# Optimization experiments

Measured on AMD Instinct MI355X. Metric: run time of the kernel, lower is better.

## Reference

```python
import jax, jax.numpy as jnp
import numpy as np

RWKV_K_CLAMP = 60.0
B, T, C = 8, 1024, 1024
LAYER_ID, N_LAYER = 2, 12


def _decay_speed():
    # replicate RWKV_TimeMix.__init__ decay_speed construction
    first = 1
    f1 = 3.0 + (LAYER_ID - first) / (N_LAYER - 1 - first) * (1.2 - 3.0)
    f2 = 0.65 + (LAYER_ID - first) / (N_LAYER - 1 - first) * (0.4 - 0.65)
    if LAYER_ID == first:
        f1 += 0.5
    if LAYER_ID == N_LAYER - 2:
        f2 = 0.4
    if LAYER_ID == N_LAYER - 1:
        f2 = 0.37
    h = np.arange(C, dtype=np.float64)
    return (f2 ** (h / (C - 1) * 7.0)) * f1


def setup_inputs() -> dict:
    key = jax.random.key(0)
    ks = jax.random.split(key, 6)
    scale = 1.0 / np.sqrt(C)
    time_mix = np.ones((C,), np.float32)
    time_mix[: C // 2] = 0.0
    return {
        "x": jax.random.normal(ks[0], (B, T, C), jnp.float32),
        "time_decay": jnp.asarray(np.log(_decay_speed()), jnp.float32),  # (C,)
        "time_first": jnp.full((C,), np.log(0.3), jnp.float32),
        "time_mix": jnp.asarray(time_mix),
        "combined_mix": jnp.full((C,), 0.01, jnp.float32),
        "Wk": jax.random.normal(ks[1], (C, C), jnp.float32) * scale,
        "Wv": jax.random.normal(ks[2], (C, C), jnp.float32) * scale,
        "Wr": jax.random.normal(ks[3], (C, C), jnp.float32) * scale,
        "Wo": jax.random.normal(ks[4], (C, C), jnp.float32) * scale,
    }


def _wkv(w, u, k, v):
    # w,u: (C,); k,v: (B,T,C). Numerically-stable decayed linear recurrence
    # (RWKV wkv kernel: running-max, like online softmax).
    b = k.shape[0]
    init = (
        jnp.zeros((b, C), k.dtype),            # numerator state a
        jnp.zeros((b, C), k.dtype),            # denominator state b
        jnp.full((b, C), -1e38, k.dtype),      # running max exponent p
    )

    def step(carry, kv):
        a, bb, p = carry
        kt, vt = kv  # (B,C)
        no = jnp.maximum(p, u + kt)
        e1 = jnp.exp(p - no)
        e2 = jnp.exp(u + kt - no)
        y = (e1 * a + e2 * vt) / (e1 * bb + e2)
        no2 = jnp.maximum(w + p, kt)
        e1 = jnp.exp(w + p - no2)
        e2 = jnp.exp(kt - no2)
        return (e1 * a + e2 * vt, e1 * bb + e2, no2), y

    _, y = jax.lax.scan(step, init, (k.transpose(1, 0, 2), v.transpose(1, 0, 2)))
    return y.transpose(1, 0, 2)  # (B,T,C)


def reference(x, time_decay, time_first, time_mix, combined_mix, Wk, Wv, Wr, Wo):
    b, t, c = x.shape
    zrow = jnp.zeros((b, 1, c), x.dtype)
    x_m1 = jnp.concatenate([zrow, x[:, :-1, :]], axis=1)   # time_shift / x_{t-1}
    x_p1 = jnp.concatenate([x[:, 1:, :], zrow], axis=1)    # x_{t+1}
    half = c // 2
    x_comb = jnp.concatenate([x_m1[:, :, :half], x_p1[:, :, half:]], axis=-1)
    xm = x * time_mix + x_m1 * (1.0 - time_mix) + x_comb * combined_mix
    k = jnp.exp(jnp.minimum(jnp.einsum("btc,dc->btd", xm, Wk), RWKV_K_CLAMP))
    v = jnp.einsum("btc,dc->btd", xm, Wv)
    r = jnp.einsum("btc,dc->btd", xm, Wr)
    wkv = _wkv(time_decay / t, time_first / t, k, v)
    return jnp.einsum("btc,dc->btd", jax.nn.sigmoid(r) * wkv, Wo)
```

## Files before the change

### kernel.cpp

```cpp
#include <hip/hip_runtime.h>
#include <hip/hip_bf16.h>
#include <stdint.h>

#define B_SZ 8
#define T_LEN 1024
#define C_DIM 1024
#define M_ROWS (B_SZ * T_LEN)
#define NCH 32
#define CHL (T_LEN / NCH)

typedef unsigned short ushort_t;
typedef __attribute__((ext_vector_type(8))) short short8;
typedef __attribute__((ext_vector_type(4))) float f32x4;
typedef __attribute__((ext_vector_type(4))) unsigned short us4;

static __device__ __forceinline__ float bf2f(ushort_t u) {
  union { unsigned int i; float f; } x; x.i = ((unsigned int)u) << 16; return x.f;
}
static __device__ __forceinline__ ushort_t f2bf(float f) {
  union { float f; unsigned int i; } x; x.f = f;
  unsigned int r = x.i + 0x7fffu + ((x.i >> 16) & 1u);
  return (ushort_t)(r >> 16);
}

static __device__ __forceinline__ void gload_lds16(const void* g, void* l) {
  __builtin_amdgcn_global_load_lds(
      (const __attribute__((address_space(1))) void*)g,
      (__attribute__((address_space(3))) void*)l, 16, 0, 0);
}

__global__ void cvt_w_kernel(const float* __restrict__ wk, const float* __restrict__ wv,
                             const float* __restrict__ wr, const float* __restrict__ wo,
                             ushort_t* __restrict__ out) {
  int gid = blockIdx.x * 256 + threadIdx.x;
  int which = gid >> 18;
  int off = (gid << 2) & ((1 << 20) - 1);
  const float* src = which == 0 ? wk : which == 1 ? wv : which == 2 ? wr : wo;
  float4 v = *(const float4*)(src + off);
  us4 o = {f2bf(v.x), f2bf(v.y), f2bf(v.z), f2bf(v.w)};
  *(us4*)(out + (size_t)gid * 4) = o;
}

__global__ void xm_kernel(const float* __restrict__ x, const float* __restrict__ tm,
                          const float* __restrict__ cm, ushort_t* __restrict__ xmb) {
  int gid = blockIdx.x * 256 + threadIdx.x;
  int c4 = (gid & (C_DIM / 4 - 1)) * 4;
  int t = (gid >> 8) & (T_LEN - 1);
  const float4 zero = {0.f, 0.f, 0.f, 0.f};
  float4 xv = *(const float4*)(x + (size_t)gid * 4);
  float4 xp = (t > 0) ? *(const float4*)(x + (size_t)gid * 4 - C_DIM) : zero;
  float4 xn = (t < T_LEN - 1) ? *(const float4*)(x + (size_t)gid * 4 + C_DIM) : zero;
  float4 tmv = *(const float4*)(tm + c4);
  float4 cmv = *(const float4*)(cm + c4);
  float4 xc = (c4 < C_DIM / 2) ? xp : xn;
  us4 o;
  o.x = f2bf(xv.x * tmv.x + xp.x * (1.f - tmv.x) + xc.x * cmv.x);
  o.y = f2bf(xv.y * tmv.y + xp.y * (1.f - tmv.y) + xc.y * cmv.y);
  o.z = f2bf(xv.z * tmv.z + xp.z * (1.f - tmv.z) + xc.z * cmv.z);
  o.w = f2bf(xv.w * tmv.w + xp.w * (1.f - tmv.w) + xc.w * cmv.w);
  *(us4*)(xmb + (size_t)gid * 4) = o;
}

__global__ __launch_bounds__(256, 3) void gemm_fused(const ushort_t* __restrict__ A,
                                                     const ushort_t* __restrict__ Bw,
                                                     ushort_t* __restrict__ outK,
                                                     ushort_t* __restrict__ outV,
                                                     ushort_t* __restrict__ outR) {
  constexpr int K = 1024;
  constexpr int NT = K / 32;
  __shared__ ushort_t As[3][128 * 32];
  __shared__ ushort_t Bs[3][128 * 32];

  const int tid = threadIdx.x;
  const int lane = tid & 63;
  const int wave = tid >> 6;

  const int bid = blockIdx.x;
  const int xcd = bid & 7;
  const int r = bid >> 3;
  const int bm = (xcd * 8 + (r & 7)) * 128;
  const int jb = r >> 3;
  const int mode = jb >> 3;
  const int bn = (jb & 7) * 128;
  const ushort_t* Bp = Bw + ((size_t)mode << 20);

  const int wr = (wave >> 1) * 64;
  const int wc = (wave & 1) * 64;

  f32x4 acc[4][4];
#pragma unroll
  for (int m = 0; m < 4; ++m)
#pragma unroll
    for (int n = 0; n < 4; ++n) acc[m][n] = (f32x4){0.f, 0.f, 0.f, 0.f};

  const int srow = tid >> 2;
  const int scol = (((tid & 3) ^ ((srow >> 1) & 3)) * 8);
  const ushort_t* Ag = A + (size_t)(bm + srow) * K + scol;
  const ushort_t* Bg = Bp + (size_t)(bn + srow) * K + scol;

  const int fr = lane & 15;
  const int kq = lane >> 4;
  const int ps = (kq ^ ((fr >> 1) & 3)) * 8;

  auto stage = [&](int buf, int k0) {
    ushort_t* ap = &As[buf][tid * 8];
    ushort_t* bp = &Bs[buf][tid * 8];
    gload_lds16(Ag + k0, ap);
    gload_lds16(Ag + (size_t)64 * K + k0, ap + 64 * 32);
    gload_lds16(Bg + k0, bp);
    gload_lds16(Bg + (size_t)64 * K + k0, bp + 64 * 32);
  };

  stage(0, 0);
  stage(1, 32);
  asm volatile("s_waitcnt vmcnt(4)" ::: "memory");
  __builtin_amdgcn_s_barrier();
  __builtin_amdgcn_sched_barrier(0);

  int cur = 0, nxt2 = 2;
#pragma unroll 1
  for (int t = 0; t < NT; ++t) {
    if (t + 2 < NT) stage(nxt2, (t + 2) * 32);
    const ushort_t* asb = &As[cur][0];
    const ushort_t* bsb = &Bs[cur][0];
    short8 af[4], bfr[4];
#pragma unroll
    for (int m = 0; m < 4; ++m)
      af[m] = *(const short8*)&asb[(wr + m * 16 + fr) * 32 + ps];
#pragma unroll
    for (int n = 0; n < 4; ++n)
      bfr[n] = *(const short8*)&bsb[(wc + n * 16 + fr) * 32 + ps];
#pragma unroll
    for (int m = 0; m < 4; ++m)
#pragma unroll
      for (int n = 0; n < 4; ++n)
        acc[m][n] = __builtin_amdgcn_mfma_f32_16x16x32_bf16(af[m], bfr[n], acc[m][n], 0, 0, 0);
    if (t + 2 < NT) {
      asm volatile("s_waitcnt vmcnt(4)" ::: "memory");
    } else {
      asm volatile("s_waitcnt vmcnt(0)" ::: "memory");
    }
    __builtin_amdgcn_s_barrier();
    __builtin_amdgcn_sched_barrier(0);
    cur = (cur == 2) ? 0 : cur + 1;
    nxt2 = (nxt2 == 2) ? 0 : nxt2 + 1;
  }

#pragma unroll
  for (int m = 0; m < 4; ++m)
#pragma unroll
    for (int n = 0; n < 4; ++n)
#pragma unroll
      for (int j = 0; j < 4; ++j) {
        float v = acc[m][n][j];
        size_t idx = (size_t)(bm + wr + m * 16 + kq * 4 + j) * C_DIM + (bn + wc + n * 16 + fr);
        if (mode == 0) {
          outK[idx] = f2bf(__expf(fminf(v, 60.f)));
        } else if (mode == 1) {
          outV[idx] = f2bf(v);
        } else {
          outR[idx] = f2bf(1.f / (1.f + __expf(-v)));
        }
      }
}

__global__ __launch_bounds__(256, 2) void gemm_out(const ushort_t* __restrict__ A,
                                                   const ushort_t* __restrict__ Bw,
                                                   float* __restrict__ outF) {
  constexpr int K = 1024;
  constexpr int NT = K / 64;
  __shared__ ushort_t As[2][128 * 64];
  __shared__ ushort_t Bs[2][128 * 64];

  const int tid = threadIdx.x;
  const int l = tid & 63;
  const int wave = tid >> 6;
  const int fr = l & 15;
  const int kq = l >> 4;

  const int bid = blockIdx.x;
  const int xcd = bid & 7;
  const int idx = bid >> 3;
  const int jb = idx >> 3;
  const int bm = (xcd * 8 + (idx & 7)) * 128;
  const int bn = jb * 128;

  const int wr = (wave >> 1) * 64;
  const int wc = (wave & 1) * 64;

  f32x4 acc[4][4];
#pragma unroll
  for (int m = 0; m < 4; ++m)
#pragma unroll
    for (int n = 0; n < 4; ++n) acc[m][n] = (f32x4){0.f, 0.f, 0.f, 0.f};

  int srow[4], scol[4];
#pragma unroll
  for (int j = 0; j < 4; ++j) {
    int row = wave * 32 + j * 8 + (l >> 3);
    srow[j] = row;
    scol[j] = ((l & 7) ^ (row & 7)) * 8;
  }
  const ushort_t* AgB = A + (size_t)bm * K;
  const ushort_t* BgB = Bw + (size_t)bn * K;
  const int dst0 = wave * 2048 + l * 8;

  auto stage = [&](int buf, int k0) {
#pragma unroll
    for (int j = 0; j < 4; ++j)
      gload_lds16(AgB + (size_t)srow[j] * K + scol[j] + k0, &As[buf][dst0 + j * 512]);
#pragma unroll
    for (int j = 0; j < 4; ++j)
      gload_lds16(BgB + (size_t)srow[j] * K + scol[j] + k0, &Bs[buf][dst0 + j * 512]);
  };

  stage(0, 0);
  asm volatile("s_waitcnt vmcnt(0)" ::: "memory");
  __syncthreads();

  const int ps0 = ((0 * 4 + kq) ^ (fr & 7)) * 8;
  const int ps1 = ((1 * 4 + kq) ^ (fr & 7)) * 8;

  int cur = 0;
  for (int t = 0; t < NT; ++t) {
    if (t < NT - 1) stage(cur ^ 1, (t + 1) * 64);
    short8 af[4][2], bfr[4][2];
#pragma unroll
    for (int m = 0; m < 4; ++m) {
      af[m][0] = *(const short8*)&As[cur][(wr + m * 16 + fr) * 64 + ps0];
      af[m][1] = *(const short8*)&As[cur][(wr + m * 16 + fr) * 64 + ps1];
    }
#pragma unroll
    for (int n = 0; n < 4; ++n) {
      bfr[n][0] = *(const short8*)&Bs[cur][(wc + n * 16 + fr) * 64 + ps0];
      bfr[n][1] = *(const short8*)&Bs[cur][(wc + n * 16 + fr) * 64 + ps1];
    }
#pragma unroll
    for (int m = 0; m < 4; ++m)
#pragma unroll
      for (int n = 0; n < 4; ++n)
#pragma unroll
        for (int ks = 0; ks < 2; ++ks)
          acc[m][n] = __builtin_amdgcn_mfma_f32_16x16x32_bf16(af[m][ks], bfr[n][ks], acc[m][n], 0, 0, 0);
    asm volatile("s_waitcnt vmcnt(0)" ::: "memory");
    __syncthreads();
    cur ^= 1;
  }

#pragma unroll
  for (int m = 0; m < 4; ++m)
#pragma unroll
    for (int n = 0; n < 4; ++n)
#pragma unroll
      for (int j = 0; j < 4; ++j)
        outF[(size_t)(bm + wr + m * 16 + kq * 4 + j) * C_DIM + (bn + wc + n * 16 + fr)] =
            acc[m][n][j];
}

__global__ void wkv_phaseA(const ushort_t* __restrict__ kk, const ushort_t* __restrict__ vv,
                           const float* __restrict__ td,
                           float* __restrict__ sa, float* __restrict__ sb,
                           float* __restrict__ sp) {
  int gid = blockIdx.x * 256 + threadIdx.x;
  int c = gid & (C_DIM - 1);
  int ch = (gid >> 10) & (NCH - 1);
  int b = gid >> 15;
  float w = td[c] * (1.f / T_LEN);
  size_t base = ((size_t)b * T_LEN + ch * CHL) * C_DIM + c;
  float a = 0.f, bb = 0.f, p = -1e38f;
  for (int t = 0; t < CHL; ++t) {
    float kt = bf2f(kk[base + (size_t)t * C_DIM]);
    float vt = bf2f(vv[base + (size_t)t * C_DIM]);
    float no2 = fmaxf(w + p, kt);
    float e1 = __expf(w + p - no2);
    float e2 = __expf(kt - no2);
    a = e1 * a + e2 * vt;
    bb = e1 * bb + e2;
    p = no2;
  }
  sa[gid] = a; sb[gid] = bb; sp[gid] = p;
}

__global__ void wkv_phaseC2(const ushort_t* __restrict__ kk, const ushort_t* __restrict__ vv,
                            const ushort_t* __restrict__ sr, const float* __restrict__ td,
                            const float* __restrict__ tf,
                            const float* __restrict__ sa, const float* __restrict__ sb,
                            const float* __restrict__ sp, ushort_t* __restrict__ sy) {
  int gid = blockIdx.x * 256 + threadIdx.x;
  int c = gid & (C_DIM - 1);
  int ch = (gid >> 10) & (NCH - 1);
  int b = gid >> 15;
  float w = td[c] * (1.f / T_LEN);
  float u = tf[c] * (1.f / T_LEN);
  float wL = w * (float)CHL;

  float a = 0.f, bb = 0.f, p = -1e38f;
  size_t sbase = ((size_t)b * NCH) * C_DIM + c;
  for (int j = 0; j < ch; ++j) {
    float ac = sa[sbase + (size_t)j * C_DIM];
    float bc = sb[sbase + (size_t)j * C_DIM];
    float pc = sp[sbase + (size_t)j * C_DIM];
    float pn = fmaxf(p + wL, pc);
    float e1 = __expf(p + wL - pn);
    float e2 = __expf(pc - pn);
    a = e1 * a + e2 * ac;
    bb = e1 * bb + e2 * bc;
    p = pn;
  }

  size_t base = ((size_t)b * T_LEN + ch * CHL) * C_DIM + c;
  for (int t = 0; t < CHL; ++t) {
    float kt = bf2f(kk[base + (size_t)t * C_DIM]);
    float vt = bf2f(vv[base + (size_t)t * C_DIM]);
    float no = fmaxf(p, u + kt);
    float e1 = __expf(p - no);
    float e2 = __expf(u + kt - no);
    float y = (e1 * a + e2 * vt) / (e1 * bb + e2);
    float srv = bf2f(sr[base + (size_t)t * C_DIM]);
    sy[base + (size_t)t * C_DIM] = f2bf(srv * y);
    float no2 = fmaxf(w + p, kt);
    e1 = __expf(w + p - no2);
    e2 = __expf(kt - no2);
    a = e1 * a + e2 * vt;
    bb = e1 * bb + e2;
    p = no2;
  }
}

extern "C" void kernel_launch(void* const* d_in, const int* in_sizes, int n_in,
                              void* d_out, int out_size, void* d_ws, size_t ws_size,
                              hipStream_t stream) {
  const float* x  = (const float*)d_in[0];
  const float* td = (const float*)d_in[1];
  const float* tf = (const float*)d_in[2];
  const float* tm = (const float*)d_in[3];
  const float* cm = (const float*)d_in[4];
  const float* Wk = (const float*)d_in[5];
  const float* Wv = (const float*)d_in[6];
  const float* Wr = (const float*)d_in[7];
  const float* Wo = (const float*)d_in[8];

  const size_t MC = (size_t)M_ROWS * C_DIM;
  const size_t CC = (size_t)C_DIM * C_DIM;

  char* ws = (char*)d_ws;
  ushort_t* xmb = (ushort_t*)ws; ws += MC * 2;
  ushort_t* Wb  = (ushort_t*)ws; ws += 4 * CC * 2;
  ushort_t* kk  = (ushort_t*)ws; ws += MC * 2;
  ushort_t* vv  = (ushort_t*)ws; ws += MC * 2;
  ushort_t* sr  = (ushort_t*)ws; ws += MC * 2;
  ushort_t* sy  = (ushort_t*)ws; ws += MC * 2;
  float* sa = (float*)ws; ws += (size_t)B_SZ * NCH * C_DIM * 4;
  float* sb = (float*)ws; ws += (size_t)B_SZ * NCH * C_DIM * 4;
  float* sp = (float*)ws; ws += (size_t)B_SZ * NCH * C_DIM * 4;

  cvt_w_kernel<<<(4 * CC / 4) / 256, 256, 0, stream>>>(Wk, Wv, Wr, Wo, Wb);
  xm_kernel<<<(MC / 4) / 256, 256, 0, stream>>>(x, tm, cm, xmb);

  gemm_fused<<<dim3(1536), 256, 0, stream>>>(xmb, Wb, kk, vv, sr);

  wkv_phaseA<<<(B_SZ * NCH * C_DIM) / 256, 256, 0, stream>>>(kk, vv, td, sa, sb, sp);
  wkv_phaseC2<<<(B_SZ * NCH * C_DIM) / 256, 256, 0, stream>>>(kk, vv, sr, td, tf, sa, sb, sp, sy);

  gemm_out<<<dim3(512), 256, 0, stream>>>(sy, Wb + 3 * CC, (float*)d_out);
}
```

Before: 153.9 us.

## Load GEMM B-operand directly to registers and merge prep kernels

Merges the weight-conversion and token-mix preprocessing kernels into one launch. In the fused KVR GEMM, the B (weight) tile is no longer staged through LDS; each wave loads its B fragments straight from global memory into double-buffered registers one k-step ahead, while A keeps a 3-stage LDS pipeline. The main loop is unrolled by six to rotate buffers statically, and launch bounds rise to 6 blocks per CU because LDS use is halved. The trade is uncoalesced per-wave global B loads with redundancy across waves, plus more register pressure, in exchange for less LDS traffic and higher occupancy.

```diff
diff --git a/kernel.cpp b/kernel.cpp
--- a/kernel.cpp
+++ b/kernel.cpp
@@ -29,47 +29,46 @@
       (__attribute__((address_space(3))) void*)l, 16, 0, 0);
 }
 
-__global__ void cvt_w_kernel(const float* __restrict__ wk, const float* __restrict__ wv,
-                             const float* __restrict__ wr, const float* __restrict__ wo,
-                             ushort_t* __restrict__ out) {
-  int gid = blockIdx.x * 256 + threadIdx.x;
-  int which = gid >> 18;
-  int off = (gid << 2) & ((1 << 20) - 1);
-  const float* src = which == 0 ? wk : which == 1 ? wv : which == 2 ? wr : wo;
-  float4 v = *(const float4*)(src + off);
-  us4 o = {f2bf(v.x), f2bf(v.y), f2bf(v.z), f2bf(v.w)};
-  *(us4*)(out + (size_t)gid * 4) = o;
-}
-
-__global__ void xm_kernel(const float* __restrict__ x, const float* __restrict__ tm,
-                          const float* __restrict__ cm, ushort_t* __restrict__ xmb) {
-  int gid = blockIdx.x * 256 + threadIdx.x;
-  int c4 = (gid & (C_DIM / 4 - 1)) * 4;
-  int t = (gid >> 8) & (T_LEN - 1);
-  const float4 zero = {0.f, 0.f, 0.f, 0.f};
-  float4 xv = *(const float4*)(x + (size_t)gid * 4);
-  float4 xp = (t > 0) ? *(const float4*)(x + (size_t)gid * 4 - C_DIM) : zero;
-  float4 xn = (t < T_LEN - 1) ? *(const float4*)(x + (size_t)gid * 4 + C_DIM) : zero;
-  float4 tmv = *(const float4*)(tm + c4);
-  float4 cmv = *(const float4*)(cm + c4);
-  float4 xc = (c4 < C_DIM / 2) ? xp : xn;
-  us4 o;
-  o.x = f2bf(xv.x * tmv.x + xp.x * (1.f - tmv.x) + xc.x * cmv.x);
-  o.y = f2bf(xv.y * tmv.y + xp.y * (1.f - tmv.y) + xc.y * cmv.y);
-  o.z = f2bf(xv.z * tmv.z + xp.z * (1.f - tmv.z) + xc.z * cmv.z);
-  o.w = f2bf(xv.w * tmv.w + xp.w * (1.f - tmv.w) + xc.w * cmv.w);
-  *(us4*)(xmb + (size_t)gid * 4) = o;
-}
-
-__global__ __launch_bounds__(256, 3) void gemm_fused(const ushort_t* __restrict__ A,
+__global__ void prep_kernel(const float* __restrict__ wk, const float* __restrict__ wv,
+                            const float* __restrict__ wr, const float* __restrict__ wo,
+                            ushort_t* __restrict__ wout,
+                            const float* __restrict__ x, const float* __restrict__ tm,
+                            const float* __restrict__ cm, ushort_t* __restrict__ xmb) {
+  if (blockIdx.x < 4096) {
+    int gid = blockIdx.x * 256 + threadIdx.x;
+    int which = gid >> 18;
+    int off = (gid << 2) & ((1 << 20) - 1);
+    const float* src = which == 0 ? wk : which == 1 ? wv : which == 2 ? wr : wo;
+    float4 v = *(const float4*)(src + off);
+    us4 o = {f2bf(v.x), f2bf(v.y), f2bf(v.z), f2bf(v.w)};
+    *(us4*)(wout + (size_t)gid * 4) = o;
+  } else {
+    int gid = (blockIdx.x - 4096) * 256 + threadIdx.x;
+    int c4 = (gid & (C_DIM / 4 - 1)) * 4;
+    int t = (gid >> 8) & (T_LEN - 1);
+    const float4 zero = {0.f, 0.f, 0.f, 0.f};
+    float4 xv = *(const float4*)(x + (size_t)gid * 4);
+    float4 xp = (t > 0) ? *(const float4*)(x + (size_t)gid * 4 - C_DIM) : zero;
+    float4 xn = (t < T_LEN - 1) ? *(const float4*)(x + (size_t)gid * 4 + C_DIM) : zero;
+    float4 tmv = *(const float4*)(tm + c4);
+    float4 cmv = *(const float4*)(cm + c4);
+    float4 xc = (c4 < C_DIM / 2) ? xp : xn;
+    us4 o;
+    o.x = f2bf(xv.x * tmv.x + xp.x * (1.f - tmv.x) + xc.x * cmv.x);
+    o.y = f2bf(xv.y * tmv.y + xp.y * (1.f - tmv.y) + xc.y * cmv.y);
+    o.z = f2bf(xv.z * tmv.z + xp.z * (1.f - tmv.z) + xc.z * cmv.z);
+    o.w = f2bf(xv.w * tmv.w + xp.w * (1.f - tmv.w) + xc.w * cmv.w);
+    *(us4*)(xmb + (size_t)gid * 4) = o;
+  }
+}
+
+__global__ __launch_bounds__(256, 6) void gemm_fused(const ushort_t* __restrict__ A,
                                                      const ushort_t* __restrict__ Bw,
                                                      ushort_t* __restrict__ outK,
                                                      ushort_t* __restrict__ outV,
                                                      ushort_t* __restrict__ outR) {
   constexpr int K = 1024;
-  constexpr int NT = K / 32;
   __shared__ ushort_t As[3][128 * 32];
-  __shared__ ushort_t Bs[3][128 * 32];
 
   const int tid = threadIdx.x;
   const int lane = tid & 63;
@@ -96,55 +95,69 @@
   const int srow = tid >> 2;
   const int scol = (((tid & 3) ^ ((srow >> 1) & 3)) * 8);
   const ushort_t* Ag = A + (size_t)(bm + srow) * K + scol;
-  const ushort_t* Bg = Bp + (size_t)(bn + srow) * K + scol;
 
   const int fr = lane & 15;
   const int kq = lane >> 4;
   const int ps = (kq ^ ((fr >> 1) & 3)) * 8;
 
-  auto stage = [&](int buf, int k0) {
+  const ushort_t* Bgl = Bp + (size_t)(bn + wc + fr) * K + kq * 8;
+
+  auto stageA = [&](int buf, int kt) {
+    const int k0 = kt * 32;
     ushort_t* ap = &As[buf][tid * 8];
-    ushort_t* bp = &Bs[buf][tid * 8];
     gload_lds16(Ag + k0, ap);
     gload_lds16(Ag + (size_t)64 * K + k0, ap + 64 * 32);
-    gload_lds16(Bg + k0, bp);
-    gload_lds16(Bg + (size_t)64 * K + k0, bp + 64 * 32);
   };
 
-  stage(0, 0);
-  stage(1, 32);
-  asm volatile("s_waitcnt vmcnt(4)" ::: "memory");
-  __builtin_amdgcn_s_barrier();
+  short8 b0[4], b1[4];
+
+#define LOADB(DST, KT)                                                        \
+  {                                                                           \
+    _Pragma("unroll") for (int n = 0; n < 4; ++n)                             \
+        DST[n] = *(const short8*)(Bgl + (size_t)n * 16 * K + (KT)*32);        \
+  }
+
+#define MFMA_STEP(ABUF, BREG)                                                 \
+  {                                                                           \
+    short8 af[4];                                                             \
+    _Pragma("unroll") for (int m = 0; m < 4; ++m)                             \
+        af[m] = *(const short8*)&As[ABUF][(wr + m * 16 + fr) * 32 + ps];      \
+    _Pragma("unroll") for (int m = 0; m < 4; ++m)                             \
+        _Pragma("unroll") for (int n = 0; n < 4; ++n)                         \
+            acc[m][n] = __builtin_amdgcn_mfma_f32_16x16x32_bf16(              \
+                af[m], BREG[n], acc[m][n], 0, 0, 0);                          \
+  }
+
+#define ENDSTEP(N)                                                            \
+  asm volatile("s_waitcnt vmcnt(" #N ")" ::: "memory");                       \
+  __builtin_amdgcn_s_barrier();                                               \
   __builtin_amdgcn_sched_barrier(0);
 
-  int cur = 0, nxt2 = 2;
+#define BODY(ACUR, ASTG, BCUR, BNXT, T)                                       \
+  LOADB(BNXT, (T) + 1);                                                       \
+  MFMA_STEP(ACUR, BCUR);                                                      \
+  stageA(ASTG, (T) + 2);                                                      \
+  ENDSTEP(2)
+
+  stageA(0, 0);
+  LOADB(b0, 0);
+  stageA(1, 1);
+  ENDSTEP(2)
+
 #pragma unroll 1
-  for (int t = 0; t < NT; ++t) {
-    if (t + 2 < NT) stage(nxt2, (t + 2) * 32);
-    const ushort_t* asb = &As[cur][0];
-    const ushort_t* bsb = &Bs[cur][0];
-    short8 af[4], bfr[4];
-#pragma unroll
-    for (int m = 0; m < 4; ++m)
-      af[m] = *(const short8*)&asb[(wr + m * 16 + fr) * 32 + ps];
-#pragma unroll
-    for (int n = 0; n < 4; ++n)
-      bfr[n] = *(const short8*)&bsb[(wc + n * 16 + fr) * 32 + ps];
-#pragma unroll
-    for (int m = 0; m < 4; ++m)
-#pragma unroll
-      for (int n = 0; n < 4; ++n)
-        acc[m][n] = __builtin_amdgcn_mfma_f32_16x16x32_bf16(af[m], bfr[n], acc[m][n], 0, 0, 0);
-    if (t + 2 < NT) {
-      asm volatile("s_waitcnt vmcnt(4)" ::: "memory");
-    } else {
-      asm volatile("s_waitcnt vmcnt(0)" ::: "memory");
-    }
-    __builtin_amdgcn_s_barrier();
-    __builtin_amdgcn_sched_barrier(0);
-    cur = (cur == 2) ? 0 : cur + 1;
-    nxt2 = (nxt2 == 2) ? 0 : nxt2 + 1;
-  }
+  for (int i = 0; i < 5; ++i) {
+    const int t0 = 6 * i;
+    BODY(0, 2, b0, b1, t0 + 0)
+    BODY(1, 0, b1, b0, t0 + 1)
+    BODY(2, 1, b0, b1, t0 + 2)
+    BODY(0, 2, b1, b0, t0 + 3)
+    BODY(1, 0, b0, b1, t0 + 4)
+    BODY(2, 1, b1, b0, t0 + 5)
+  }
+  LOADB(b1, 31);
+  MFMA_STEP(0, b0);
+  ENDSTEP(0)
+  MFMA_STEP(1, b1);
 
 #pragma unroll
   for (int m = 0; m < 4; ++m)
@@ -162,6 +175,10 @@
           outR[idx] = f2bf(1.f / (1.f + __expf(-v)));
         }
       }
+#undef BODY
+#undef ENDSTEP
+#undef MFMA_STEP
+#undef LOADB
 }
 
 __global__ __launch_bounds__(256, 2) void gemm_out(const ushort_t* __restrict__ A,
@@ -354,8 +371,7 @@
   float* sb = (float*)ws; ws += (size_t)B_SZ * NCH * C_DIM * 4;
   float* sp = (float*)ws; ws += (size_t)B_SZ * NCH * C_DIM * 4;
 
-  cvt_w_kernel<<<(4 * CC / 4) / 256, 256, 0, stream>>>(Wk, Wv, Wr, Wo, Wb);
-  xm_kernel<<<(MC / 4) / 256, 256, 0, stream>>>(x, tm, cm, xmb);
+  prep_kernel<<<dim3(12288), 256, 0, stream>>>(Wk, Wv, Wr, Wo, Wb, x, tm, cm, xmb);
 
   gemm_fused<<<dim3(1536), 256, 0, stream>>>(xmb, Wb, kk, vv, sr);
 
```

New measurement: 494.5 us. +221.3%, slower.
